# Kernel optimization log

Hardware: AMD Instinct MI355X
Metric: run time of the kernel (lower is better)

## Reference

```python
import jax, jax.numpy as jnp
import numpy as np

N = 256
MAX_LENGTH = 1024
BATCH = 32768


def _transition(n):
    # HiPPO-LegS transition matrices (float64 numpy, matches torch module)
    q = np.arange(n, dtype=np.float64)
    col, row = np.meshgrid(q, q)
    r = 2 * q + 1
    M = -(np.where(row >= col, r, 0) - np.diag(q))
    T = np.sqrt(np.diag(2 * q + 1))
    A = T @ M @ np.linalg.inv(T)
    B = np.diag(T)  # squeezed (N,)
    return A, B


def _build_stacked(n, max_length):
    # Bilinear (Tustin) discretization at every timescale t=1..max_length.
    A, B = _transition(n)
    ts = np.arange(1, max_length + 1, dtype=np.float64)  # (L,)
    At = A[None] / ts[:, None, None]                     # (L,N,N)
    Bt = B[None] / ts[:, None]                           # (L,N)
    I = np.eye(n)
    lhs = I[None] - At / 2                               # (L,N,N), lower triangular
    A_stacked = np.linalg.solve(lhs, I[None] + At / 2)   # (L,N,N)
    B_stacked = np.linalg.solve(lhs, Bt[..., None])[..., 0]  # (L,N)
    return A_stacked.astype(np.float32), B_stacked.astype(np.float32)


def setup_inputs() -> dict:
    key = jax.random.key(0)
    k1, k2 = jax.random.split(key)
    A_np, B_np = _build_stacked(N, MAX_LENGTH)
    return {
        "c": jax.random.normal(k1, (BATCH, N), dtype=jnp.float32),
        "f": jax.random.normal(k2, (BATCH, 1), dtype=jnp.float32),
        "A_stacked": jnp.asarray(A_np),  # (L, N, N) buffer
        "B_stacked": jnp.asarray(B_np),  # (L, N) buffer
        "t": 512,
    }


def reference(c, f, A_stacked, B_stacked, t):
    # F.linear(c, A) == c @ A.T ; then scaled add of new value f
    A = A_stacked[t]            # (N, N)
    b = B_stacked[t]            # (N,)
    return c @ A.T + b * f      # (BATCH, N)
```

## Files before the change

kernel.cpp:

```cpp
#include <hip/hip_runtime.h>
#include <cstdint>
#include <cstddef>

typedef _Float16 half8 __attribute__((ext_vector_type(8)));
typedef float f32x4 __attribute__((ext_vector_type(4)));

static constexpr int kN  = 256;
static constexpr int kBM = 64;
static constexpr size_t kHalfB  = 64 * 1024;
static constexpr size_t kLDS    = kHalfB;

__global__ __launch_bounds__(256) void hippo_prep(
    const float* __restrict__ A_stacked, const int* __restrict__ tptr,
    _Float16* __restrict__ a16)
{
    const int t = tptr[0];
    const float* __restrict__ A = A_stacked + (size_t)t * kN * kN;
    const int tid = blockIdx.x * 256 + threadIdx.x;
    const int ksh = tid >> 12;
    const int nt  = (tid >> 8) & 15;
    const int ks2 = (tid >> 6) & 3;
    const int l   = tid & 63;
    const int row = nt * 16 + (l & 15);
    const int k0  = (ksh * 4 + ks2) * 32 + ((l >> 4) << 3);
    const float* __restrict__ src = A + (size_t)row * kN + k0;
    f32x4 v0 = *(const f32x4*)(src);
    f32x4 v1 = *(const f32x4*)(src + 4);
    half8 h;
    h[0] = (_Float16)v0[0]; h[1] = (_Float16)v0[1];
    h[2] = (_Float16)v0[2]; h[3] = (_Float16)v0[3];
    h[4] = (_Float16)v1[0]; h[5] = (_Float16)v1[1];
    h[6] = (_Float16)v1[2]; h[7] = (_Float16)v1[3];
    ((half8*)a16)[tid] = h;
}

__global__ __launch_bounds__(256, 2) void hippo_gemm(
    const float* __restrict__ c, const float* __restrict__ f,
    const float* __restrict__ Bst, const int* __restrict__ tptr,
    const _Float16* __restrict__ a16, float* __restrict__ out)
{
    extern __shared__ char lds_raw[];

    const int tid  = threadIdx.x;
    const int l    = tid & 63;
    const int wid  = tid >> 6;
    const int lo16 = l & 15;
    const int hi4  = l >> 4;
    const int bid  = blockIdx.x;
    const int m0   = bid * kBM + wid * 16;
    const int hA   = bid & 1;
    const int hB   = hA ^ 1;

    const char* __restrict__ gsrcA = (const char*)a16 + (size_t)hA * kHalfB;
    #pragma unroll
    for (int i = 0; i < 16; ++i) {
        const size_t off = (size_t)(i * 4 + wid) * 1024 + (size_t)l * 16;
        __builtin_amdgcn_global_load_lds(
            (const __attribute__((address_space(1))) void*)(gsrcA + off),
            (__attribute__((address_space(3))) void*)(lds_raw + off),
            16, 0, 0);
    }

    const float* __restrict__ cptr = c + (size_t)(m0 + lo16) * kN + (hi4 << 3);
    f32x4 cv0[4], cv1[4];
    #pragma unroll
    for (int ks = 0; ks < 4; ++ks) {
        cv0[ks] = *(const f32x4*)(cptr + hA * 128 + ks * 32);
        cv1[ks] = *(const f32x4*)(cptr + hA * 128 + ks * 32 + 4);
    }

    const int t = tptr[0];
    const float* __restrict__ brow = Bst + (size_t)t * kN;
    float bvs[16];
    #pragma unroll
    for (int nt = 0; nt < 16; ++nt) bvs[nt] = brow[nt * 16 + lo16];
    float fv[4];
    #pragma unroll
    for (int r = 0; r < 4; ++r) fv[r] = f[m0 + (hi4 << 2) + r];

    __syncthreads();

    half8 af[4];
    #pragma unroll
    for (int ks = 0; ks < 4; ++ks) {
        af[ks][0] = (_Float16)cv0[ks][0]; af[ks][1] = (_Float16)cv0[ks][1];
        af[ks][2] = (_Float16)cv0[ks][2]; af[ks][3] = (_Float16)cv0[ks][3];
        af[ks][4] = (_Float16)cv1[ks][0]; af[ks][5] = (_Float16)cv1[ks][1];
        af[ks][6] = (_Float16)cv1[ks][2]; af[ks][7] = (_Float16)cv1[ks][3];
    }

    f32x4 dv0[4], dv1[4];
    #pragma unroll
    for (int ks = 0; ks < 4; ++ks) {
        dv0[ks] = *(const f32x4*)(cptr + hB * 128 + ks * 32);
        dv1[ks] = *(const f32x4*)(cptr + hB * 128 + ks * 32 + 4);
    }

    const half8* __restrict__ Bs = (const half8*)lds_raw;
    f32x4 acc[16];
    #pragma unroll
    for (int i = 0; i < 16; ++i) acc[i] = (f32x4){0.f, 0.f, 0.f, 0.f};
    #pragma unroll
    for (int ks = 0; ks < 4; ++ks) {
        #pragma unroll
        for (int nt = 0; nt < 16; ++nt) {
            half8 bf = Bs[(nt * 4 + ks) * 64 + l];
            acc[nt] = __builtin_amdgcn_mfma_f32_16x16x32_f16(af[ks], bf, acc[nt], 0, 0, 0);
        }
    }

    __syncthreads();

    const char* __restrict__ gsrcB = (const char*)a16 + (size_t)hB * kHalfB;
    #pragma unroll
    for (int i = 0; i < 16; ++i) {
        const size_t off = (size_t)(i * 4 + wid) * 1024 + (size_t)l * 16;
        __builtin_amdgcn_global_load_lds(
            (const __attribute__((address_space(1))) void*)(gsrcB + off),
            (__attribute__((address_space(3))) void*)(lds_raw + off),
            16, 0, 0);
    }
    half8 ag[4];
    #pragma unroll
    for (int ks = 0; ks < 4; ++ks) {
        ag[ks][0] = (_Float16)dv0[ks][0]; ag[ks][1] = (_Float16)dv0[ks][1];
        ag[ks][2] = (_Float16)dv0[ks][2]; ag[ks][3] = (_Float16)dv0[ks][3];
        ag[ks][4] = (_Float16)dv1[ks][0]; ag[ks][5] = (_Float16)dv1[ks][1];
        ag[ks][6] = (_Float16)dv1[ks][2]; ag[ks][7] = (_Float16)dv1[ks][3];
    }

    __syncthreads();

    float* __restrict__ obase = out + (size_t)(m0 + (hi4 << 2)) * kN + lo16;
    #pragma unroll
    for (int nt = 0; nt < 16; ++nt) {
        f32x4 a = acc[nt];
        #pragma unroll
        for (int ks = 0; ks < 4; ++ks) {
            half8 bf = Bs[(nt * 4 + ks) * 64 + l];
            a = __builtin_amdgcn_mfma_f32_16x16x32_f16(ag[ks], bf, a, 0, 0, 0);
        }
        #pragma unroll
        for (int r = 0; r < 4; ++r)
            obase[(size_t)r * kN + nt * 16] = a[r] + bvs[nt] * fv[r];
    }
}

extern "C" void kernel_launch(void* const* d_in, const int* in_sizes, int n_in,
                              void* d_out, int out_size, void* d_ws, size_t ws_size,
                              hipStream_t stream) {
    const float* c   = (const float*)d_in[0];
    const float* f   = (const float*)d_in[1];
    const float* A   = (const float*)d_in[2];
    const float* B   = (const float*)d_in[3];
    const int*   t   = (const int*)d_in[4];
    float* out = (float*)d_out;
    _Float16* a16 = (_Float16*)d_ws;

    const int batch = in_sizes[0] / kN;

    hipFuncSetAttribute((const void*)hippo_gemm,
                        hipFuncAttributeMaxDynamicSharedMemorySize,
                        (int)kLDS);

    hipLaunchKernelGGL(hippo_prep, dim3(32), dim3(256), 0, stream, A, t, a16);
    hipLaunchKernelGGL(hippo_gemm, dim3(batch / kBM), dim3(256), kLDS, stream,
                       c, f, B, t, a16, out);
}
```

Before: 22.68 us.

## Skip zero upper-triangular tiles of the lower-triangular transition matrix in GEMM

The GEMM now exploits the lower-triangular structure of the HiPPO-LegS discretized matrix. It skips MFMA tiles and LDS loads for k-blocks above the diagonal, and it drops the per-block half-swap ordering so that every block processes the upper K-half first and then the lower half. This removes roughly 40% of the MFMAs and the A-tile traffic. The cost is that correctness now depends on A being lower triangular, which is a structural property of the buffer rather than of arbitrary inputs. It also makes the loads and MFMA work uneven across waves.

Result: faster. 22.08 us (median of 3 runs) (-2.7%).

```diff
diff --git a/kernel.cpp b/kernel.cpp
--- a/kernel.cpp
+++ b/kernel.cpp
@@ -48,25 +48,27 @@
     const int hi4  = l >> 4;
     const int bid  = blockIdx.x;
     const int m0   = bid * kBM + wid * 16;
-    const int hA   = bid & 1;
-    const int hB   = hA ^ 1;
 
-    const char* __restrict__ gsrcA = (const char*)a16 + (size_t)hA * kHalfB;
+    const char* __restrict__ gsrc1 = (const char*)a16 + kHalfB;
     #pragma unroll
-    for (int i = 0; i < 16; ++i) {
-        const size_t off = (size_t)(i * 4 + wid) * 1024 + (size_t)l * 16;
-        __builtin_amdgcn_global_load_lds(
-            (const __attribute__((address_space(1))) void*)(gsrcA + off),
-            (__attribute__((address_space(3))) void*)(lds_raw + off),
-            16, 0, 0);
+    for (int j = 0; j < 4; ++j) {
+        const int nt = wid + j * 4;
+        const int kmax = (nt - 8) >> 1;
+        for (int ks2 = 0; ks2 <= kmax && ks2 < 4; ++ks2) {
+            const size_t off = (size_t)(nt * 4 + ks2) * 1024 + (size_t)l * 16;
+            __builtin_amdgcn_global_load_lds(
+                (const __attribute__((address_space(1))) void*)(gsrc1 + off),
+                (__attribute__((address_space(3))) void*)(lds_raw + off),
+                16, 0, 0);
+        }
     }
 
     const float* __restrict__ cptr = c + (size_t)(m0 + lo16) * kN + (hi4 << 3);
     f32x4 cv0[4], cv1[4];
     #pragma unroll
     for (int ks = 0; ks < 4; ++ks) {
-        cv0[ks] = *(const f32x4*)(cptr + hA * 128 + ks * 32);
-        cv1[ks] = *(const f32x4*)(cptr + hA * 128 + ks * 32 + 4);
+        cv0[ks] = *(const f32x4*)(cptr + 128 + ks * 32);
+        cv1[ks] = *(const f32x4*)(cptr + 128 + ks * 32 + 4);
     }
 
     const int t = tptr[0];
@@ -92,8 +94,8 @@
     f32x4 dv0[4], dv1[4];
     #pragma unroll
     for (int ks = 0; ks < 4; ++ks) {
-        dv0[ks] = *(const f32x4*)(cptr + hB * 128 + ks * 32);
-        dv1[ks] = *(const f32x4*)(cptr + hB * 128 + ks * 32 + 4);
+        dv0[ks] = *(const f32x4*)(cptr + ks * 32);
+        dv1[ks] = *(const f32x4*)(cptr + ks * 32 + 4);
     }
 
     const half8* __restrict__ Bs = (const half8*)lds_raw;
@@ -101,24 +103,30 @@
     #pragma unroll
     for (int i = 0; i < 16; ++i) acc[i] = (f32x4){0.f, 0.f, 0.f, 0.f};
     #pragma unroll
-    for (int ks = 0; ks < 4; ++ks) {
+    for (int ks2 = 0; ks2 < 4; ++ks2) {
         #pragma unroll
         for (int nt = 0; nt < 16; ++nt) {
-            half8 bf = Bs[(nt * 4 + ks) * 64 + l];
-            acc[nt] = __builtin_amdgcn_mfma_f32_16x16x32_f16(af[ks], bf, acc[nt], 0, 0, 0);
+            if (nt >= 8 + 2 * ks2) {
+                half8 bf = Bs[(nt * 4 + ks2) * 64 + l];
+                acc[nt] = __builtin_amdgcn_mfma_f32_16x16x32_f16(af[ks2], bf, acc[nt], 0, 0, 0);
+            }
         }
     }
 
     __syncthreads();
 
-    const char* __restrict__ gsrcB = (const char*)a16 + (size_t)hB * kHalfB;
+    const char* __restrict__ gsrc0 = (const char*)a16;
     #pragma unroll
-    for (int i = 0; i < 16; ++i) {
-        const size_t off = (size_t)(i * 4 + wid) * 1024 + (size_t)l * 16;
-        __builtin_amdgcn_global_load_lds(
-            (const __attribute__((address_space(1))) void*)(gsrcB + off),
-            (__attribute__((address_space(3))) void*)(lds_raw + off),
-            16, 0, 0);
+    for (int j = 0; j < 4; ++j) {
+        const int nt = wid + j * 4;
+        const int kmax = nt >> 1;
+        for (int ks2 = 0; ks2 <= kmax && ks2 < 4; ++ks2) {
+            const size_t off = (size_t)(nt * 4 + ks2) * 1024 + (size_t)l * 16;
+            __builtin_amdgcn_global_load_lds(
+                (const __attribute__((address_space(1))) void*)(gsrc0 + off),
+                (__attribute__((address_space(3))) void*)(lds_raw + off),
+                16, 0, 0);
+        }
     }
     half8 ag[4];
     #pragma unroll
@@ -136,9 +144,11 @@
     for (int nt = 0; nt < 16; ++nt) {
         f32x4 a = acc[nt];
         #pragma unroll
-        for (int ks = 0; ks < 4; ++ks) {
-            half8 bf = Bs[(nt * 4 + ks) * 64 + l];
-            a = __builtin_amdgcn_mfma_f32_16x16x32_f16(ag[ks], bf, a, 0, 0, 0);
+        for (int ks2 = 0; ks2 < 4; ++ks2) {
+            if (ks2 <= (nt >> 1)) {
+                half8 bf = Bs[(nt * 4 + ks2) * 64 + l];
+                a = __builtin_amdgcn_mfma_f32_16x16x32_f16(ag[ks2], bf, a, 0, 0, 0);
+            }
         }
         #pragma unroll
         for (int r = 0; r < 4; ++r)
```
